# Kernel optimization log

Measured on AMD Instinct MI355X. Metric: run time of the kernel, lower is better.

Reference implementation:

```python
import jax, jax.numpy as jnp
import numpy as np

N_NODES = 4096
IN_FEAT = 256
N_HEADS = 8
N_HIDDEN = 64  # out_features // n_heads
NEG_SLOPE = 0.2
EDGE_PROB = 0.05


def setup_inputs() -> dict:
    key = jax.random.key(0)
    k1, k2, k3, k4 = jax.random.split(key, 4)
    h = jax.random.normal(k1, (N_NODES, IN_FEAT), dtype=jnp.float32)
    # binary adjacency mask [N, N, 1] (broadcast over heads), as in the torch asserts
    adj_mat = (jax.random.uniform(k2, (N_NODES, N_NODES, 1)) < EDGE_PROB).astype(jnp.float32)
    # nn.Linear(in_features, n_heads*n_hidden, bias=False) weight: [H*F, in]
    W = jax.random.normal(k3, (N_HEADS * N_HIDDEN, IN_FEAT), dtype=jnp.float32) / np.sqrt(IN_FEAT)
    # nn.Linear(2*n_hidden, 1, bias=False) weight, flattened: [2*F]
    a = jax.random.normal(k4, (2 * N_HIDDEN,), dtype=jnp.float32) / np.sqrt(2 * N_HIDDEN)
    return {"h": h, "adj_mat": adj_mat, "W": W, "a": a}


def reference(h, adj_mat, W, a):
    n = h.shape[0]
    # g: [N, H, F]
    g = (h @ W.T).reshape(n, N_HEADS, N_HIDDEN)
    # attn(cat[g_i, g_j]) == a_l . g_i + a_r . g_j  (linear, no bias)
    a_l = a[:N_HIDDEN]
    a_r = a[N_HIDDEN:]
    el = jnp.einsum('ihf,f->ih', g, a_l)  # [N, H]
    er = jnp.einsum('jhf,f->jh', g, a_r)  # [N, H]
    e = jax.nn.leaky_relu(el[:, None, :] + er[None, :, :], NEG_SLOPE)  # [N, N, H]
    # note: original multiplies scores by adjacency (not masked_fill)
    e = e * adj_mat  # adj broadcasts over heads
    att = jax.nn.softmax(e, axis=1)  # softmax over source nodes j
    # dropout is identity at eval (dropout_rate=0.0)
    out = jnp.einsum('ijh,jhf->ihf', att, g)  # [N, H, F]
    return out.reshape(n, N_HEADS * N_HIDDEN)
```

## Files before the change

### kernel.cpp

```cpp
#include <hip/hip_runtime.h>
#include <float.h>

#define N_NODES 4096
#define IN_FEAT 256
#define N_HEADS 8
#define N_HIDDEN 64
#define OUT_FEAT (N_HEADS * N_HIDDEN)
#define MAXE 512
#define NEG_SLOPE 0.2f
#define KC 128

typedef _Float16 half8 __attribute__((ext_vector_type(8)));
typedef _Float16 half2v __attribute__((ext_vector_type(2)));
typedef float floatx4 __attribute__((ext_vector_type(4)));

__device__ inline unsigned fkey(float f) {
  unsigned u = __float_as_uint(f);
  return (u & 0x80000000u) ? ~u : (u | 0x80000000u);
}
__device__ inline float fkey_inv(unsigned k) {
  unsigned u = (k & 0x80000000u) ? (k & 0x7fffffffu) : ~k;
  return __uint_as_float(u);
}

__global__ __launch_bounds__(256, 2) void gemm_fused(
    const float* __restrict__ H, const float* __restrict__ Wt,
    const float* __restrict__ a,
    _Float16* __restrict__ G16, float* __restrict__ el, float* __restrict__ er,
    float* __restrict__ gsum, unsigned* __restrict__ ermax_keys) {
  __shared__ _Float16 Ah[64 * KC];
  __shared__ _Float16 Al[64 * KC];
  __shared__ _Float16 Bh[64 * KC];
  __shared__ _Float16 Bl[64 * KC];
  const int t = threadIdx.x;
  const int w = t >> 6, l = t & 63;
  const int n16 = l & 15, q = l >> 4;
  const int bi = blockIdx.x, bo = blockIdx.y;
  const int m0 = bi * 64 + w * 16;

  floatx4 acc[4];
#pragma unroll
  for (int ct = 0; ct < 4; ++ct) acc[ct] = (floatx4)0.f;

  for (int kc = 0; kc < 2; ++kc) {
    if (kc) __syncthreads();
#pragma unroll
    for (int p = 0; p < 8; ++p) {
      const int idx = p * 256 + t;
      const int r = idx >> 5;
      const int c4 = (idx & 31) << 2;
      const int dst = r * KC + (((idx & 31) >> 1) ^ (r & 7)) * 8 + (idx & 1) * 4;
      float4 hv = *(const float4*)(H + (size_t)(bi * 64 + r) * IN_FEAT + kc * KC + c4);
      float4 wv = *(const float4*)(Wt + (size_t)(bo * 64 + r) * IN_FEAT + kc * KC + c4);
      union { _Float16 h[4]; int2 d; } hh_, hl_, wh_, wl_;
      hh_.h[0] = (_Float16)hv.x; hh_.h[1] = (_Float16)hv.y;
      hh_.h[2] = (_Float16)hv.z; hh_.h[3] = (_Float16)hv.w;
      hl_.h[0] = (_Float16)(hv.x - (float)hh_.h[0]);
      hl_.h[1] = (_Float16)(hv.y - (float)hh_.h[1]);
      hl_.h[2] = (_Float16)(hv.z - (float)hh_.h[2]);
      hl_.h[3] = (_Float16)(hv.w - (float)hh_.h[3]);
      wh_.h[0] = (_Float16)wv.x; wh_.h[1] = (_Float16)wv.y;
      wh_.h[2] = (_Float16)wv.z; wh_.h[3] = (_Float16)wv.w;
      wl_.h[0] = (_Float16)(wv.x - (float)wh_.h[0]);
      wl_.h[1] = (_Float16)(wv.y - (float)wh_.h[1]);
      wl_.h[2] = (_Float16)(wv.z - (float)wh_.h[2]);
      wl_.h[3] = (_Float16)(wv.w - (float)wh_.h[3]);
      *(int2*)&Ah[dst] = hh_.d;
      *(int2*)&Al[dst] = hl_.d;
      *(int2*)&Bh[dst] = wh_.d;
      *(int2*)&Bl[dst] = wl_.d;
    }
    __syncthreads();
#pragma unroll
    for (int ks = 0; ks < 4; ++ks) {
      const int aoff = (w * 16 + n16) * KC + (((ks << 2) + q) ^ (n16 & 7)) * 8;
      half8 Afh = *(const half8*)&Ah[aoff];
      half8 Afl = *(const half8*)&Al[aoff];
#pragma unroll
      for (int ct = 0; ct < 4; ++ct) {
        const int boff = (ct * 16 + n16) * KC + (((ks << 2) + q) ^ (n16 & 7)) * 8;
        half8 Bfh = *(const half8*)&Bh[boff];
        half8 Bfl = *(const half8*)&Bl[boff];
        acc[ct] = __builtin_amdgcn_mfma_f32_16x16x32_f16(Afh, Bfh, acc[ct], 0, 0, 0);
        acc[ct] = __builtin_amdgcn_mfma_f32_16x16x32_f16(Afl, Bfh, acc[ct], 0, 0, 0);
        acc[ct] = __builtin_amdgcn_mfma_f32_16x16x32_f16(Afh, Bfl, acc[ct], 0, 0, 0);
      }
    }
  }

  float aLv[4], aRv[4];
#pragma unroll
  for (int ct = 0; ct < 4; ++ct) {
    aLv[ct] = a[ct * 16 + n16];
    aRv[ct] = a[64 + ct * 16 + n16];
  }

  float erv[4];
#pragma unroll
  for (int reg = 0; reg < 4; ++reg) {
    float sl = 0.f, sr = 0.f;
#pragma unroll
    for (int ct = 0; ct < 4; ++ct) {
      sl = fmaf(acc[ct][reg], aLv[ct], sl);
      sr = fmaf(acc[ct][reg], aRv[ct], sr);
    }
#pragma unroll
    for (int off = 1; off < 16; off <<= 1) {
      sl += __shfl_xor(sl, off);
      sr += __shfl_xor(sr, off);
    }
    erv[reg] = sr;
    if (n16 == 0) {
      const int rowi = m0 + q * 4 + reg;
      el[(size_t)rowi * N_HEADS + bo] = sl;
      er[(size_t)rowi * N_HEADS + bo] = sr;
    }
  }

  {
    float mx = fmaxf(fmaxf(erv[0], erv[1]), fmaxf(erv[2], erv[3]));
    mx = fmaxf(mx, __shfl_xor(mx, 16));
    mx = fmaxf(mx, __shfl_xor(mx, 32));
    if (l == 0) atomicMax(ermax_keys + bo, fkey(mx));
  }

#pragma unroll
  for (int ct = 0; ct < 4; ++ct) {
    float s = acc[ct][0] + acc[ct][1] + acc[ct][2] + acc[ct][3];
    s += __shfl_xor(s, 16);
    s += __shfl_xor(s, 32);
    if (l < 16) atomicAdd(gsum + bo * 64 + ct * 16 + n16, s);
  }

  __syncthreads();
  _Float16* LG = Ah;
#pragma unroll
  for (int ct = 0; ct < 4; ++ct)
#pragma unroll
    for (int reg = 0; reg < 4; ++reg)
      LG[(w * 16 + q * 4 + reg) * 72 + ct * 16 + n16] = (_Float16)acc[ct][reg];
  __syncthreads();
  {
    const int row = t >> 2, ch = t & 3;
    int4 v0 = *(const int4*)&LG[row * 72 + ch * 16];
    int4 v1 = *(const int4*)&LG[row * 72 + ch * 16 + 8];
    _Float16* dst = G16 + (size_t)(bi * 64 + row) * OUT_FEAT + bo * 64 + ch * 16;
    *(int4*)dst = v0;
    *(int4*)(dst + 8) = v1;
  }
}

__global__ __launch_bounds__(256, 8) void attn_sparse(
    const float* __restrict__ adj, const _Float16* __restrict__ G16,
    const float* __restrict__ el, const float* __restrict__ er,
    const unsigned* __restrict__ ermax_keys, const float* __restrict__ gsum,
    float* __restrict__ out) {
  __shared__ int jlist[MAXE];
  __shared__ _Float16 w16[MAXE * N_HEADS];
  __shared__ float accp[4][OUT_FEAT];
  __shared__ float el_s[N_HEADS], ermax_s[N_HEADS];
  __shared__ float zw[4][N_HEADS];
  __shared__ float em_s[N_HEADS], invz_s[N_HEADS];
  __shared__ int cnt;

  const int i = blockIdx.x;
  const int t = threadIdx.x;
  if (t == 0) cnt = 0;
  if (t < N_HEADS) {
    el_s[t] = el[(size_t)i * N_HEADS + t];
    ermax_s[t] = fkey_inv(ermax_keys[t]);
  }
  __syncthreads();

  const float* row = adj + (size_t)i * N_NODES;
#pragma unroll
  for (int q = 0; q < 4; ++q) {
    int j0 = (q * 256 + t) * 4;
    float4 v = *(const float4*)(row + j0);
    if (v.x != 0.f) { int p = atomicAdd(&cnt, 1); if (p < MAXE) jlist[p] = j0; }
    if (v.y != 0.f) { int p = atomicAdd(&cnt, 1); if (p < MAXE) jlist[p] = j0 + 1; }
    if (v.z != 0.f) { int p = atomicAdd(&cnt, 1); if (p < MAXE) jlist[p] = j0 + 2; }
    if (v.w != 0.f) { int p = atomicAdd(&cnt, 1); if (p < MAXE) jlist[p] = j0 + 3; }
  }
  __syncthreads();
  const int deg = min(cnt, MAXE);

  const int h2 = t & 7;
  const float m_h = fmaxf(0.f, el_s[h2] + ermax_s[h2]);
  const float em_h = __expf(-m_h);
  float zacc = 0.f;
  for (int jj = t >> 3; jj < deg; jj += 32) {
    int j = jlist[jj];
    float x = el_s[h2] + er[(size_t)j * N_HEADS + h2];
    x = fmaxf(x, NEG_SLOPE * x);
    float wv = __expf(x - m_h);
    zacc += wv;
    w16[jj * N_HEADS + h2] = (_Float16)wv;
  }
#pragma unroll
  for (int off = 8; off < 64; off <<= 1) zacc += __shfl_xor(zacc, off);
  if ((t & 63) < 8) zw[t >> 6][t & 7] = zacc;
  __syncthreads();
  if (t < 8) {
    float Z = zw[0][t] + zw[1][t] + zw[2][t] + zw[3][t] +
              (float)(N_NODES - deg) * em_h;
    invz_s[t] = 1.f / Z;
    em_s[t] = em_h;
  }

  const int wv4 = t >> 6;
  const int hh = (t >> 3) & 7;
  const int lq = t & 7;
  const float m_hh = fmaxf(0.f, el_s[hh] + ermax_s[hh]);
  const float em = __expf(-m_hh);
  const _Float16 em16 = (_Float16)em;
  float accf[8];
#pragma unroll
  for (int k = 0; k < 8; ++k) accf[k] = 0.f;

  if (deg > 0) {
    const int last = deg - 1;
    _Float16 c0 = (_Float16)0.f, c1 = (_Float16)0.f;
    half8 g0, g1;
    {
      const int e0 = wv4, e1 = wv4 + 4;
      int ja = jlist[min(e0, last)];
      int jb = jlist[min(e1, last)];
      if (e0 < deg) c0 = w16[e0 * N_HEADS + hh] - em16;
      if (e1 < deg) c1 = w16[e1 * N_HEADS + hh] - em16;
      g0 = *(const half8*)(G16 + (size_t)ja * OUT_FEAT + hh * 64 + lq * 8);
      g1 = *(const half8*)(G16 + (size_t)jb * OUT_FEAT + hh * 64 + lq * 8);
    }
    for (int base = 0; base < deg; base += 8) {
      _Float16 cn0 = (_Float16)0.f, cn1 = (_Float16)0.f;
      half8 gn0 = g0, gn1 = g1;
      if (base + 8 < deg) {
        const int n0 = base + 8 + wv4, n1 = base + 12 + wv4;
        int ja = jlist[min(n0, last)];
        int jb = jlist[min(n1, last)];
        if (n0 < deg) cn0 = w16[n0 * N_HEADS + hh] - em16;
        if (n1 < deg) cn1 = w16[n1 * N_HEADS + hh] - em16;
        gn0 = *(const half8*)(G16 + (size_t)ja * OUT_FEAT + hh * 64 + lq * 8);
        gn1 = *(const half8*)(G16 + (size_t)jb * OUT_FEAT + hh * 64 + lq * 8);
      }
#if __has_builtin(__builtin_amdgcn_fdot2)
      {
        half2v c2 = {c0, c1};
#pragma unroll
        for (int d = 0; d < 4; ++d) {
          half2v blo = {g0[2 * d], g1[2 * d]};
          half2v bhi = {g0[2 * d + 1], g1[2 * d + 1]};
          accf[2 * d] = __builtin_amdgcn_fdot2(c2, blo, accf[2 * d], false);
          accf[2 * d + 1] = __builtin_amdgcn_fdot2(c2, bhi, accf[2 * d + 1], false);
        }
      }
#else
      {
        const float f0 = (float)c0, f1 = (float)c1;
#pragma unroll
        for (int k = 0; k < 8; ++k) {
          accf[k] = fmaf(f0, (float)g0[k], accf[k]);
          accf[k] = fmaf(f1, (float)g1[k], accf[k]);
        }
      }
#endif
      c0 = cn0; c1 = cn1; g0 = gn0; g1 = gn1;
    }
  }
  {
    float4 a0 = make_float4(accf[0], accf[1], accf[2], accf[3]);
    float4 a1 = make_float4(accf[4], accf[5], accf[6], accf[7]);
    *(float4*)&accp[wv4][hh * 64 + lq * 8] = a0;
    *(float4*)&accp[wv4][hh * 64 + lq * 8 + 4] = a1;
  }
  __syncthreads();

  {
    const int c0 = t * 2;
    const int hf = c0 >> 6;
    float2 s = make_float2(0.f, 0.f);
#pragma unroll
    for (int g = 0; g < 4; ++g) {
      float2 p = *(const float2*)&accp[g][c0];
      s.x += p.x; s.y += p.y;
    }
    float2 gs = *(const float2*)(gsum + c0);
    const float emf = em_s[hf], iz = invz_s[hf];
    float2 o = make_float2((s.x + emf * gs.x) * iz, (s.y + emf * gs.y) * iz);
    *(float2*)(out + (size_t)i * OUT_FEAT + c0) = o;
  }
}

extern "C" void kernel_launch(void* const* d_in, const int* in_sizes, int n_in,
                              void* d_out, int out_size, void* d_ws, size_t ws_size,
                              hipStream_t stream) {
  const float* h   = (const float*)d_in[0];
  const float* adj = (const float*)d_in[1];
  const float* W   = (const float*)d_in[2];
  const float* a   = (const float*)d_in[3];
  float* out = (float*)d_out;

  char* ws = (char*)d_ws;
  _Float16* G16        = (_Float16*)ws;
  float*    el         = (float*)(ws + 4u * 1024 * 1024);
  float*    er         = (float*)(ws + 4u * 1024 * 1024 + 128 * 1024);
  float*    gsum       = (float*)(ws + 4u * 1024 * 1024 + 256 * 1024);
  unsigned* ermax_keys = (unsigned*)(ws + 4u * 1024 * 1024 + 258 * 1024);

  hipMemsetAsync(gsum, 0, 2048 + 32, stream);
  gemm_fused<<<dim3(64, 8), 256, 0, stream>>>(h, W, a, G16, el, er, gsum, ermax_keys);
  attn_sparse<<<dim3(N_NODES), 256, 0, stream>>>(adj, G16, el, er, ermax_keys, gsum, out);
}
```

Baseline: 174.3 us.

## Replace sparse gather attention with dense MFMA attention over adjacency bitmask

Adds a pass that packs the float adjacency matrix into 64-bit ballot bitmasks. The sparse per-row gather attention is replaced by a dense tiled kernel: each block computes a 64x64 tile of probabilities per head, choosing the exp score or the non-edge constant from the bitmask, and multiplies it with a transposed fp16 G tile using MFMA. G, el and er are now stored transposed by head. The gsum atomics and the sparse edge lists go away, at the cost of full dense N^2 exp and matmul work plus an extra kernel launch and a bitmask pass over adj.

```diff
diff --git a/kernel.cpp b/kernel.cpp
--- a/kernel.cpp
+++ b/kernel.cpp
@@ -6,12 +6,10 @@
 #define N_HEADS 8
 #define N_HIDDEN 64
 #define OUT_FEAT (N_HEADS * N_HIDDEN)
-#define MAXE 512
 #define NEG_SLOPE 0.2f
 #define KC 128
 
 typedef _Float16 half8 __attribute__((ext_vector_type(8)));
-typedef _Float16 half2v __attribute__((ext_vector_type(2)));
 typedef float floatx4 __attribute__((ext_vector_type(4)));
 
 __device__ inline unsigned fkey(float f) {
@@ -23,11 +21,23 @@
   return __uint_as_float(u);
 }
 
+__global__ __launch_bounds__(256) void adj2bits(const float* __restrict__ adj,
+                                                unsigned long long* __restrict__ bits) {
+  const int t = threadIdx.x;
+#pragma unroll
+  for (int it = 0; it < 4; ++it) {
+    size_t gid = (size_t)it * (16384u * 256u) + (size_t)blockIdx.x * 256 + t;
+    float v = adj[gid];
+    unsigned long long m = __ballot(v != 0.f);
+    if ((t & 63) == 0) bits[gid >> 6] = m;
+  }
+}
+
 __global__ __launch_bounds__(256, 2) void gemm_fused(
     const float* __restrict__ H, const float* __restrict__ Wt,
     const float* __restrict__ a,
-    _Float16* __restrict__ G16, float* __restrict__ el, float* __restrict__ er,
-    float* __restrict__ gsum, unsigned* __restrict__ ermax_keys) {
+    _Float16* __restrict__ GT16, float* __restrict__ elT, float* __restrict__ erT,
+    unsigned* __restrict__ ermax_keys) {
   __shared__ _Float16 Ah[64 * KC];
   __shared__ _Float16 Al[64 * KC];
   __shared__ _Float16 Bh[64 * KC];
@@ -94,7 +104,6 @@
     aLv[ct] = a[ct * 16 + n16];
     aRv[ct] = a[64 + ct * 16 + n16];
   }
-
   float erv[4];
 #pragma unroll
   for (int reg = 0; reg < 4; ++reg) {
@@ -112,11 +121,10 @@
     erv[reg] = sr;
     if (n16 == 0) {
       const int rowi = m0 + q * 4 + reg;
-      el[(size_t)rowi * N_HEADS + bo] = sl;
-      er[(size_t)rowi * N_HEADS + bo] = sr;
-    }
-  }
-
+      elT[(size_t)bo * N_NODES + rowi] = sl;
+      erT[(size_t)bo * N_NODES + rowi] = sr;
+    }
+  }
   {
     float mx = fmaxf(fmaxf(erv[0], erv[1]), fmaxf(erv[2], erv[3]));
     mx = fmaxf(mx, __shfl_xor(mx, 16));
@@ -124,14 +132,6 @@
     if (l == 0) atomicMax(ermax_keys + bo, fkey(mx));
   }
 
-#pragma unroll
-  for (int ct = 0; ct < 4; ++ct) {
-    float s = acc[ct][0] + acc[ct][1] + acc[ct][2] + acc[ct][3];
-    s += __shfl_xor(s, 16);
-    s += __shfl_xor(s, 32);
-    if (l < 16) atomicAdd(gsum + bo * 64 + ct * 16 + n16, s);
-  }
-
   __syncthreads();
   _Float16* LG = Ah;
 #pragma unroll
@@ -141,153 +141,113 @@
       LG[(w * 16 + q * 4 + reg) * 72 + ct * 16 + n16] = (_Float16)acc[ct][reg];
   __syncthreads();
   {
-    const int row = t >> 2, ch = t & 3;
-    int4 v0 = *(const int4*)&LG[row * 72 + ch * 16];
-    int4 v1 = *(const int4*)&LG[row * 72 + ch * 16 + 8];
-    _Float16* dst = G16 + (size_t)(bi * 64 + row) * OUT_FEAT + bo * 64 + ch * 16;
-    *(int4*)dst = v0;
-    *(int4*)(dst + 8) = v1;
-  }
-}
-
-__global__ __launch_bounds__(256, 8) void attn_sparse(
-    const float* __restrict__ adj, const _Float16* __restrict__ G16,
-    const float* __restrict__ el, const float* __restrict__ er,
-    const unsigned* __restrict__ ermax_keys, const float* __restrict__ gsum,
-    float* __restrict__ out) {
-  __shared__ int jlist[MAXE];
-  __shared__ _Float16 w16[MAXE * N_HEADS];
-  __shared__ float accp[4][OUT_FEAT];
-  __shared__ float el_s[N_HEADS], ermax_s[N_HEADS];
-  __shared__ float zw[4][N_HEADS];
-  __shared__ float em_s[N_HEADS], invz_s[N_HEADS];
-  __shared__ int cnt;
-
-  const int i = blockIdx.x;
+    const int f = t >> 2, jq = t & 3;
+    union { _Float16 hh[16]; int4 v[2]; } u;
+#pragma unroll
+    for (int k = 0; k < 16; ++k) u.hh[k] = LG[(jq * 16 + k) * 72 + f];
+    _Float16* dst = GT16 + (size_t)(bo * 64 + f) * N_NODES + bi * 64 + jq * 16;
+    *(int4*)dst = u.v[0];
+    *(int4*)(dst + 8) = u.v[1];
+  }
+}
+
+__global__ __launch_bounds__(256, 2) void attn_dense2(
+    const unsigned long long* __restrict__ bits, const _Float16* __restrict__ GT16,
+    const float* __restrict__ elT, const float* __restrict__ erT,
+    const unsigned* __restrict__ ermax_keys, float* __restrict__ out) {
+  __shared__ _Float16 P[64 * 64];
+  __shared__ _Float16 Gt[2][64 * 64];
+  __shared__ float ers[2][64];
+  __shared__ float els[64], ms[64], ems[64], Zs[64];
+
   const int t = threadIdx.x;
-  if (t == 0) cnt = 0;
-  if (t < N_HEADS) {
-    el_s[t] = el[(size_t)i * N_HEADS + t];
-    ermax_s[t] = fkey_inv(ermax_keys[t]);
-  }
-  __syncthreads();
-
-  const float* row = adj + (size_t)i * N_NODES;
-#pragma unroll
-  for (int q = 0; q < 4; ++q) {
-    int j0 = (q * 256 + t) * 4;
-    float4 v = *(const float4*)(row + j0);
-    if (v.x != 0.f) { int p = atomicAdd(&cnt, 1); if (p < MAXE) jlist[p] = j0; }
-    if (v.y != 0.f) { int p = atomicAdd(&cnt, 1); if (p < MAXE) jlist[p] = j0 + 1; }
-    if (v.z != 0.f) { int p = atomicAdd(&cnt, 1); if (p < MAXE) jlist[p] = j0 + 2; }
-    if (v.w != 0.f) { int p = atomicAdd(&cnt, 1); if (p < MAXE) jlist[p] = j0 + 3; }
-  }
-  __syncthreads();
-  const int deg = min(cnt, MAXE);
-
-  const int h2 = t & 7;
-  const float m_h = fmaxf(0.f, el_s[h2] + ermax_s[h2]);
-  const float em_h = __expf(-m_h);
+  const int ib = blockIdx.x, h = blockIdx.y;
+  const int i0 = ib * 64;
+  const int pi = t >> 2, pj = t & 3;
+  const int w = t >> 6, n16 = t & 15, q = (t & 63) >> 4;
+
+  if (t < 64) {
+    float e = elT[(size_t)h * N_NODES + i0 + t];
+    float m = fmaxf(0.f, e + fkey_inv(ermax_keys[h]));
+    els[t] = e; ms[t] = m; ems[t] = __expf(-m);
+    ers[0][t] = erT[(size_t)h * N_NODES + t];
+  }
+  {
+    const int sf = t >> 2, sseg = t & 3;
+    const _Float16* src = GT16 + (size_t)(h * 64 + sf) * N_NODES + sseg * 16;
+    int4 v0 = *(const int4*)src;
+    int4 v1 = *(const int4*)(src + 8);
+    *(int4*)&Gt[0][sf * 64 + ((sseg * 2) ^ (sf & 7)) * 8] = v0;
+    *(int4*)&Gt[0][sf * 64 + ((sseg * 2 + 1) ^ (sf & 7)) * 8] = v1;
+  }
+  __syncthreads();
+
+  const float el_i = els[pi], m_i = ms[pi], em_i = ems[pi];
+  const unsigned long long* brow = bits + (size_t)(i0 + pi) * 64;
   float zacc = 0.f;
-  for (int jj = t >> 3; jj < deg; jj += 32) {
-    int j = jlist[jj];
-    float x = el_s[h2] + er[(size_t)j * N_HEADS + h2];
-    x = fmaxf(x, NEG_SLOPE * x);
-    float wv = __expf(x - m_h);
-    zacc += wv;
-    w16[jj * N_HEADS + h2] = (_Float16)wv;
-  }
-#pragma unroll
-  for (int off = 8; off < 64; off <<= 1) zacc += __shfl_xor(zacc, off);
-  if ((t & 63) < 8) zw[t >> 6][t & 7] = zacc;
-  __syncthreads();
-  if (t < 8) {
-    float Z = zw[0][t] + zw[1][t] + zw[2][t] + zw[3][t] +
-              (float)(N_NODES - deg) * em_h;
-    invz_s[t] = 1.f / Z;
-    em_s[t] = em_h;
-  }
-
-  const int wv4 = t >> 6;
-  const int hh = (t >> 3) & 7;
-  const int lq = t & 7;
-  const float m_hh = fmaxf(0.f, el_s[hh] + ermax_s[hh]);
-  const float em = __expf(-m_hh);
-  const _Float16 em16 = (_Float16)em;
-  float accf[8];
-#pragma unroll
-  for (int k = 0; k < 8; ++k) accf[k] = 0.f;
-
-  if (deg > 0) {
-    const int last = deg - 1;
-    _Float16 c0 = (_Float16)0.f, c1 = (_Float16)0.f;
-    half8 g0, g1;
+
+  floatx4 acc[4];
+#pragma unroll
+  for (int ft = 0; ft < 4; ++ft) acc[ft] = (floatx4)0.f;
+
+  int par = 0;
+  for (int s = 0; s < 64; ++s) {
     {
-      const int e0 = wv4, e1 = wv4 + 4;
-      int ja = jlist[min(e0, last)];
-      int jb = jlist[min(e1, last)];
-      if (e0 < deg) c0 = w16[e0 * N_HEADS + hh] - em16;
-      if (e1 < deg) c1 = w16[e1 * N_HEADS + hh] - em16;
-      g0 = *(const half8*)(G16 + (size_t)ja * OUT_FEAT + hh * 64 + lq * 8);
-      g1 = *(const half8*)(G16 + (size_t)jb * OUT_FEAT + hh * 64 + lq * 8);
-    }
-    for (int base = 0; base < deg; base += 8) {
-      _Float16 cn0 = (_Float16)0.f, cn1 = (_Float16)0.f;
-      half8 gn0 = g0, gn1 = g1;
-      if (base + 8 < deg) {
-        const int n0 = base + 8 + wv4, n1 = base + 12 + wv4;
-        int ja = jlist[min(n0, last)];
-        int jb = jlist[min(n1, last)];
-        if (n0 < deg) cn0 = w16[n0 * N_HEADS + hh] - em16;
-        if (n1 < deg) cn1 = w16[n1 * N_HEADS + hh] - em16;
-        gn0 = *(const half8*)(G16 + (size_t)ja * OUT_FEAT + hh * 64 + lq * 8);
-        gn1 = *(const half8*)(G16 + (size_t)jb * OUT_FEAT + hh * 64 + lq * 8);
+      const unsigned long long bv = brow[s];
+      union { _Float16 hh[16]; int4 v[2]; } up;
+      float z0 = 0.f;
+#pragma unroll
+      for (int k = 0; k < 16; ++k) {
+        const int jl = pj * 16 + k;
+        float x = el_i + ers[par][jl];
+        x = fmaxf(x, NEG_SLOPE * x);
+        float p = __expf(x - m_i);
+        float sel = ((bv >> jl) & 1ull) ? p : em_i;
+        z0 += sel;
+        up.hh[k] = (_Float16)sel;
       }
-#if __has_builtin(__builtin_amdgcn_fdot2)
-      {
-        half2v c2 = {c0, c1};
-#pragma unroll
-        for (int d = 0; d < 4; ++d) {
-          half2v blo = {g0[2 * d], g1[2 * d]};
-          half2v bhi = {g0[2 * d + 1], g1[2 * d + 1]};
-          accf[2 * d] = __builtin_amdgcn_fdot2(c2, blo, accf[2 * d], false);
-          accf[2 * d + 1] = __builtin_amdgcn_fdot2(c2, bhi, accf[2 * d + 1], false);
-        }
+      zacc += z0;
+      *(int4*)&P[pi * 64 + ((pj * 2) ^ (pi & 7)) * 8] = up.v[0];
+      *(int4*)&P[pi * 64 + ((pj * 2 + 1) ^ (pi & 7)) * 8] = up.v[1];
+    }
+    __syncthreads();
+    if (s + 1 < 64) {
+      const int sf = t >> 2, sseg = t & 3;
+      const _Float16* src = GT16 + (size_t)(h * 64 + sf) * N_NODES + (s + 1) * 64 + sseg * 16;
+      int4 v0 = *(const int4*)src;
+      int4 v1 = *(const int4*)(src + 8);
+      *(int4*)&Gt[par ^ 1][sf * 64 + ((sseg * 2) ^ (sf & 7)) * 8] = v0;
+      *(int4*)&Gt[par ^ 1][sf * 64 + ((sseg * 2 + 1) ^ (sf & 7)) * 8] = v1;
+      if (t < 64) ers[par ^ 1][t] = erT[(size_t)h * N_NODES + (s + 1) * 64 + t];
+    }
+#pragma unroll
+    for (int ks = 0; ks < 2; ++ks) {
+      half8 Af = *(const half8*)&P[(w * 16 + n16) * 64 + (((ks << 2) + q) ^ (n16 & 7)) * 8];
+#pragma unroll
+      for (int ft = 0; ft < 4; ++ft) {
+        half8 Bf = *(const half8*)&Gt[par][(ft * 16 + n16) * 64 + (((ks << 2) + q) ^ (n16 & 7)) * 8];
+        acc[ft] = __builtin_amdgcn_mfma_f32_16x16x32_f16(Af, Bf, acc[ft], 0, 0, 0);
       }
-#else
-      {
-        const float f0 = (float)c0, f1 = (float)c1;
-#pragma unroll
-        for (int k = 0; k < 8; ++k) {
-          accf[k] = fmaf(f0, (float)g0[k], accf[k]);
-          accf[k] = fmaf(f1, (float)g1[k], accf[k]);
-        }
-      }
-#endif
-      c0 = cn0; c1 = cn1; g0 = gn0; g1 = gn1;
-    }
-  }
-  {
-    float4 a0 = make_float4(accf[0], accf[1], accf[2], accf[3]);
-    float4 a1 = make_float4(accf[4], accf[5], accf[6], accf[7]);
-    *(float4*)&accp[wv4][hh * 64 + lq * 8] = a0;
-    *(float4*)&accp[wv4][hh * 64 + lq * 8 + 4] = a1;
-  }
-  __syncthreads();
-
-  {
-    const int c0 = t * 2;
-    const int hf = c0 >> 6;
-    float2 s = make_float2(0.f, 0.f);
-#pragma unroll
-    for (int g = 0; g < 4; ++g) {
-      float2 p = *(const float2*)&accp[g][c0];
-      s.x += p.x; s.y += p.y;
-    }
-    float2 gs = *(const float2*)(gsum + c0);
-    const float emf = em_s[hf], iz = invz_s[hf];
-    float2 o = make_float2((s.x + emf * gs.x) * iz, (s.y + emf * gs.y) * iz);
-    *(float2*)(out + (size_t)i * OUT_FEAT + c0) = o;
+    }
+    __syncthreads();
+    par ^= 1;
+  }
+
+  {
+    float z = zacc;
+    z += __shfl_xor(z, 1);
+    z += __shfl_xor(z, 2);
+    if (pj == 0) Zs[pi] = z;
+  }
+  __syncthreads();
+
+#pragma unroll
+  for (int reg = 0; reg < 4; ++reg) {
+    const int il = w * 16 + q * 4 + reg;
+    const float iz = 1.f / Zs[il];
+    float* op = out + (size_t)(i0 + il) * OUT_FEAT + h * 64;
+#pragma unroll
+    for (int ft = 0; ft < 4; ++ft) op[ft * 16 + n16] = acc[ft][reg] * iz;
   }
 }
 
@@ -301,13 +261,14 @@
   float* out = (float*)d_out;
 
   char* ws = (char*)d_ws;
-  _Float16* G16        = (_Float16*)ws;
-  float*    el         = (float*)(ws + 4u * 1024 * 1024);
-  float*    er         = (float*)(ws + 4u * 1024 * 1024 + 128 * 1024);
-  float*    gsum       = (float*)(ws + 4u * 1024 * 1024 + 256 * 1024);
-  unsigned* ermax_keys = (unsigned*)(ws + 4u * 1024 * 1024 + 258 * 1024);
-
-  hipMemsetAsync(gsum, 0, 2048 + 32, stream);
-  gemm_fused<<<dim3(64, 8), 256, 0, stream>>>(h, W, a, G16, el, er, gsum, ermax_keys);
-  attn_sparse<<<dim3(N_NODES), 256, 0, stream>>>(adj, G16, el, er, ermax_keys, gsum, out);
-}
+  _Float16* GT16 = (_Float16*)ws;
+  unsigned long long* bits = (unsigned long long*)(ws + 4u * 1024 * 1024);
+  float* elT = (float*)(ws + 6u * 1024 * 1024);
+  float* erT = (float*)(ws + 6u * 1024 * 1024 + 128 * 1024);
+  unsigned* ermax_keys = (unsigned*)(ws + 6u * 1024 * 1024 + 256 * 1024);
+
+  hipMemsetAsync(ermax_keys, 0, 32, stream);
+  adj2bits<<<dim3(16384), 256, 0, stream>>>(adj, bits);
+  gemm_fused<<<dim3(64, 8), 256, 0, stream>>>(h, W, a, GT16, elT, erT, ermax_keys);
+  attn_dense2<<<dim3(64, 8), 256, 0, stream>>>(bits, GT16, elT, erT, ermax_keys, out);
+}
```

Result: slower. 233.8 us (+34.2%).
